# Kernel optimization log

Hardware: AMD Instinct MI355X
Metric: run time of the kernel (lower is better)

The kernel has to match this reference:

```python
import jax, jax.numpy as jnp
import numpy as np
from jax import lax

EPS = 1e-5  # BatchNorm3d default eps


def _dwconv3d(x, w, pad):
    # x: [N,C,D,H,W], w: [C,1,k,k,k] depthwise kernel
    C = w.shape[0]
    return lax.conv_general_dilated(
        x, w,
        window_strides=(1, 1, 1),
        padding=[(pad, pad)] * 3,
        dimension_numbers=('NCDHW', 'OIDHW', 'NCDHW'),
        feature_group_count=C,
    )


def _bn_relu(y, gamma, beta, mean, var):
    # Inference-mode BatchNorm3d folded into a per-channel affine, then ReLU.
    inv = gamma / jnp.sqrt(var + EPS)          # [C]
    scale = inv.reshape(1, -1, 1, 1, 1)
    bias = (beta - mean * inv).reshape(1, -1, 1, 1, 1)
    return jax.nn.relu(y * scale + bias)


def setup_inputs() -> dict:
    key = jax.random.key(0)
    ks = jax.random.split(key, 20)
    C = 32
    x = jax.random.normal(ks[0], (2, C, 64, 128, 128), dtype=jnp.float32)
    w7 = jax.random.normal(ks[1], (C, 1, 7, 7, 7), dtype=jnp.float32) * 0.05
    w3 = jax.random.normal(ks[2], (C, 1, 3, 3, 3), dtype=jnp.float32) * 0.1
    w1 = jax.random.normal(ks[3], (C, 1, 1, 1, 1), dtype=jnp.float32) * 0.3
    def bn_params(i):
        g = jax.random.normal(ks[4 + 4 * i], (C,), dtype=jnp.float32) * 0.1 + 1.0
        b = jax.random.normal(ks[5 + 4 * i], (C,), dtype=jnp.float32) * 0.1
        m = jax.random.normal(ks[6 + 4 * i], (C,), dtype=jnp.float32) * 0.1
        v = jax.random.uniform(ks[7 + 4 * i], (C,), dtype=jnp.float32) + 0.5
        return g, b, m, v
    g7, b7, m7, v7 = bn_params(0)
    g3, b3, m3, v3 = bn_params(1)
    g1, b1, m1, v1 = bn_params(2)
    return dict(x=x, w7=w7, w3=w3, w1=w1,
                g7=g7, b7=b7, m7=m7, v7=v7,
                g3=g3, b3=b3, m3=m3, v3=v3,
                g1=g1, b1=b1, m1=m1, v1=v1)


def reference(x, w7, w3, w1,
              g7, b7, m7, v7,
              g3, b3, m3, v3,
              g1, b1, m1, v1):
    # y = relu(bn7(dw7(x))) + relu(bn3(dw3(x))) + relu(bn1(dw1(x)))
    y = _bn_relu(_dwconv3d(x, w7, 3), g7, b7, m7, v7)
    y = y + _bn_relu(_dwconv3d(x, w3, 1), g3, b3, m3, v3)
    # 1x1x1 depthwise conv == per-channel scalar multiply
    y = y + _bn_relu(x * w1[:, 0, 0, 0, 0].reshape(1, -1, 1, 1, 1), g1, b1, m1, v1)
    return jax.nn.relu(x + y)
```

## Files before the change

kernel.cpp:

```cpp
#include <hip/hip_runtime.h>
#include <hip/hip_bf16.h>

#define Dd 64
#define Hh 128
#define Ww 128
#define Cc 32

#define BD 32
#define BH 16
#define BW 16
#define ZR (BD + 6)
#define HR (BH + 6)
#define NR (ZR * HR)
#define RCOLS 24
#define BLKROW 3
#define NBLK (NR * BLKROW)

#define N7WIN 14
#define N3WIN 10
#define W3BASE (49 * N7WIN)
#define ZENT   (W3BASE + 9 * N3WIN)
#define NENT   (ZENT + 1)

typedef __attribute__((ext_vector_type(8))) short short8;
typedef __attribute__((ext_vector_type(4))) float floatx4;

static __device__ __forceinline__ unsigned short f2bf(float f) {
    unsigned u = __builtin_bit_cast(unsigned, f);
    u += 0x7fffu + ((u >> 16) & 1u);
    return (unsigned short)(u >> 16);
}

static __device__ __forceinline__ unsigned pk2(float a, float b) {
    union { __hip_bfloat162 h; unsigned u; } cv;
    cv.h = __float22bfloat162_rn(make_float2(a, b));
    return cv.u;
}

__global__ __launch_bounds__(256, 3) void replk_mfma(
    const float* __restrict__ x,
    const float* __restrict__ w7, const float* __restrict__ w3, const float* __restrict__ w1,
    const float* __restrict__ g7, const float* __restrict__ b7, const float* __restrict__ m7, const float* __restrict__ v7,
    const float* __restrict__ g3, const float* __restrict__ b3, const float* __restrict__ m3, const float* __restrict__ v3,
    const float* __restrict__ g1, const float* __restrict__ b1, const float* __restrict__ m1, const float* __restrict__ v1,
    float* __restrict__ out)
{
    __shared__ __align__(16) unsigned short tile[NR * RCOLS];
    __shared__ __align__(16) unsigned short wtab[NENT * 8];

    const int tid = threadIdx.x;

    const unsigned lid = blockIdx.x;
    const unsigned nl = (lid & 7u) * 1024u + (lid >> 3);
    const int bx = nl & 127;
    const int slab = nl >> 7;
    const int c = slab & 31;
    const int nb = slab >> 5;
    const int w0 = (bx & 7) * BW;
    const int h0 = ((bx >> 3) & 7) * BH;
    const int d0 = (bx >> 6) * BD;

    const float* xc = x + (size_t)(nb * Cc + c) * (Dd * Hh * Ww);

    for (int e = tid; e < NENT; e += 256) {
        unsigned short h8[8];
#pragma unroll
        for (int j = 0; j < 8; j++) {
            float v = 0.f;
            if (e < W3BASE) {
                int pl = e / N7WIN, a = e - pl * N7WIN;
                int t = a + j - 7;
                if ((unsigned)t < 7u)
                    v = w7[c * 343 + (pl / 7) * 49 + (pl % 7) * 7 + t];
            } else if (e < ZENT) {
                int e2 = e - W3BASE;
                int p3 = e2 / N3WIN, a = e2 - p3 * N3WIN;
                int t = a + j - 7;
                if ((unsigned)t < 3u)
                    v = w3[c * 27 + (p3 / 3) * 9 + (p3 % 3) * 3 + t];
            }
            h8[j] = f2bf(v);
        }
        uint4 pk;
        pk.x = (unsigned)h8[0] | ((unsigned)h8[1] << 16);
        pk.y = (unsigned)h8[2] | ((unsigned)h8[3] << 16);
        pk.z = (unsigned)h8[4] | ((unsigned)h8[5] << 16);
        pk.w = (unsigned)h8[6] | ((unsigned)h8[7] << 16);
        *(uint4*)&wtab[e * 8] = pk;
    }

#pragma unroll
    for (int it = 0; it < 10; it++) {
        int s = tid + it * 256;
        if (s < NBLK) {
            int R = s / BLKROW, bl = s - R * BLKROW;
            int zi = R / HR, hr = R - zi * HR;
            int gz = d0 - 3 + zi, gh = h0 - 3 + hr, gw0 = w0 - 4 + bl * 8;
            float v[8];
#pragma unroll
            for (int j = 0; j < 8; j++) v[j] = 0.f;
            if ((unsigned)gz < (unsigned)Dd && (unsigned)gh < (unsigned)Hh) {
                const float* src = xc + ((size_t)gz * Hh + gh) * Ww + gw0;
                if (gw0 >= 0 && gw0 + 8 <= Ww) {
                    float4 a = *(const float4*)src;
                    float4 b = *(const float4*)(src + 4);
                    v[0] = a.x; v[1] = a.y; v[2] = a.z; v[3] = a.w;
                    v[4] = b.x; v[5] = b.y; v[6] = b.z; v[7] = b.w;
                } else {
#pragma unroll
                    for (int j = 0; j < 8; j++) {
                        int gw = gw0 + j;
                        if ((unsigned)gw < (unsigned)Ww) v[j] = src[j];
                    }
                }
            }
            uint4 pk;
            pk.x = pk2(v[0], v[1]);
            pk.y = pk2(v[2], v[3]);
            pk.z = pk2(v[4], v[5]);
            pk.w = pk2(v[6], v[7]);
            *(uint4*)&tile[R * RCOLS + bl * 8] = pk;
        }
    }

    const float eps = 1e-5f;
    const float iv7 = g7[c] / sqrtf(v7[c] + eps);
    const float bb7 = b7[c] - m7[c] * iv7;
    const float iv3 = g3[c] / sqrtf(v3[c] + eps);
    const float bb3 = b3[c] - m3[c] * iv3;
    const float iv1 = g1[c] / sqrtf(v1[c] + eps);
    const float bb1 = b1[c] - m1[c] * iv1;
    const float s1 = w1[c] * iv1;

    __syncthreads();

    const int lane = tid & 63;
    const int wave = tid >> 6;
    const int q = lane & 15;
    const int p = lane >> 4;
    const int khp = p >> 1;
    const int kb  = p & 1;
    const int ddl = q >> 3;
    const int mwq = q & 7;
    const int zbase = wave * 8;

    const int a7 = 8 * kb - mwq + 6;
    const int a3 = a7 - 2;
    const short8* wf = (const short8*)wtab;

    floatx4 acc7[4][2], acc3[4][2];
#pragma unroll
    for (int i = 0; i < 4; i++)
#pragma unroll
        for (int wh = 0; wh < 2; wh++) { acc7[i][wh] = (floatx4)0.f; acc3[i][wh] = (floatx4)0.f; }

#pragma unroll 1
    for (int khg = 0; khg < 4; khg++) {
        const int kh = 2 * khg + khp;
        const bool ok7 = ((unsigned)a7 < 14u) && (kh <= 6);
        const int cb7 = ok7 ? (kh * 14 + a7 - ddl * 98) : (int)ZENT;
        const int st7 = ok7 ? 98 : 0;
        short8 A7g[8];
#pragma unroll
        for (int rz = 0; rz < 8; rz++) {
            int idx = cb7 + rz * st7;
            if (rz == 0) idx = (ddl == 0 && ok7) ? idx : (int)ZENT;
            if (rz == 7) idx = (ddl == 1 && ok7) ? idx : (int)ZENT;
            A7g[rz] = wf[idx];
        }

        const bool has3 = (khg == 1) || (khg == 2);
        short8 A3g[4] = {};
        if (has3) {
            const int kh3 = 2 * (khg - 1) + khp;
            const bool ok3 = ((unsigned)a3 < 10u) && (kh3 <= 2);
            const int cb3 = ok3 ? (W3BASE + kh3 * 10 + a3 - ddl * 30) : (int)ZENT;
            const int st3 = ok3 ? 30 : 0;
#pragma unroll
            for (int rz = 0; rz < 4; rz++) {
                int idx = cb3 + rz * st3;
                if (rz == 0) idx = (ddl == 0 && ok3) ? idx : (int)ZENT;
                if (rz == 3) idx = (ddl == 1 && ok3) ? idx : (int)ZENT;
                A3g[rz] = wf[idx];
            }
        }

        const int rowadd = (khg == 3) ? 6 : (2 * khg + khp);

#pragma unroll
        for (int zi = 0; zi < 14; zi++) {
            const int R = (zbase + zi) * HR + q + rowadd;
            const unsigned short* bp = &tile[R * RCOLS + 8 * kb];
            short8 B0 = *(const short8*)bp;
            short8 B1 = *(const short8*)(bp + 8);
#pragma unroll
            for (int ddg = 0; ddg < 4; ddg++) {
                const int rz = zi - 2 * ddg;
                if (rz >= 0 && rz < 8) {
                    acc7[ddg][0] = __builtin_amdgcn_mfma_f32_16x16x32_bf16(
                        A7g[rz], B0, acc7[ddg][0], 0, 0, 0);
                    acc7[ddg][1] = __builtin_amdgcn_mfma_f32_16x16x32_bf16(
                        A7g[rz], B1, acc7[ddg][1], 0, 0, 0);
                }
            }
            if (has3) {
#pragma unroll
                for (int ddg = 0; ddg < 4; ddg++) {
                    const int rz3 = zi - 2 - 2 * ddg;
                    if (rz3 >= 0 && rz3 < 4) {
                        acc3[ddg][0] = __builtin_amdgcn_mfma_f32_16x16x32_bf16(
                            A3g[rz3], B0, acc3[ddg][0], 0, 0, 0);
                        acc3[ddg][1] = __builtin_amdgcn_mfma_f32_16x16x32_bf16(
                            A3g[rz3], B1, acc3[ddg][1], 0, 0, 0);
                    }
                }
            }
        }
    }

#pragma unroll
    for (int ddg = 0; ddg < 4; ddg++) {
#pragma unroll
        for (int wh = 0; wh < 2; wh++) {
            const int d = d0 + zbase + 2 * ddg + khp;
            const int Rr = (zbase + 2 * ddg + khp + 3) * HR + (q + 3);
            uint2 u = *(const uint2*)&tile[Rr * RCOLS + 8 * wh + 4 * kb + 4];
            float xr[4];
            xr[0] = __builtin_bit_cast(float, u.x << 16);
            xr[1] = __builtin_bit_cast(float, u.x & 0xffff0000u);
            xr[2] = __builtin_bit_cast(float, u.y << 16);
            xr[3] = __builtin_bit_cast(float, u.y & 0xffff0000u);

            size_t off = ((size_t)(nb * Cc + c) * Dd + d) * (Hh * Ww)
                       + (size_t)(h0 + q) * Ww + w0 + 8 * wh + 4 * kb;
            float o[4];
#pragma unroll
            for (int r = 0; r < 4; r++) {
                float y7 = fmaxf(fmaf(acc7[ddg][wh][r], iv7, bb7), 0.f);
                float y3 = fmaxf(fmaf(acc3[ddg][wh][r], iv3, bb3), 0.f);
                float y1 = fmaxf(fmaf(xr[r], s1, bb1), 0.f);
                o[r] = fmaxf(xr[r] + y7 + y3 + y1, 0.f);
            }
            *(float4*)(out + off) = make_float4(o[0], o[1], o[2], o[3]);
        }
    }
}

extern "C" void kernel_launch(void* const* d_in, const int* in_sizes, int n_in,
                              void* d_out, int out_size, void* d_ws, size_t ws_size,
                              hipStream_t stream) {
    const float* x  = (const float*)d_in[0];
    const float* w7 = (const float*)d_in[1];
    const float* w3 = (const float*)d_in[2];
    const float* w1 = (const float*)d_in[3];
    const float* g7 = (const float*)d_in[4];
    const float* b7 = (const float*)d_in[5];
    const float* m7 = (const float*)d_in[6];
    const float* v7 = (const float*)d_in[7];
    const float* g3 = (const float*)d_in[8];
    const float* b3 = (const float*)d_in[9];
    const float* m3 = (const float*)d_in[10];
    const float* v3 = (const float*)d_in[11];
    const float* g1 = (const float*)d_in[12];
    const float* b1 = (const float*)d_in[13];
    const float* m1 = (const float*)d_in[14];
    const float* v1 = (const float*)d_in[15];
    float* out = (float*)d_out;

    dim3 grid(8192);
    dim3 block(256);
    hipLaunchKernelGGL(replk_mfma, grid, block, 0, stream,
                       x, w7, w3, w1, g7, b7, m7, v7, g3, b3, m3, v3,
                       g1, b1, m1, v1, out);
}
```

Baseline: 260.2 us.

## Split width halves across waves with 512-thread blocks

Doubles the block to 512 threads and splits the two 8-wide column halves of each output tile across separate waves, so each wave keeps half the accumulators and loads one B fragment per row instead of two. The halo tile and weight-table fills use the larger thread count, which shortens the load loops. This cuts register pressure per wave and raises parallelism and occupancy. In exchange, every wave redundantly loads the A weight fragments, and there are more waves per block to schedule around the barrier.

```diff
diff --git a/kernel.cpp b/kernel.cpp
--- a/kernel.cpp
+++ b/kernel.cpp
@@ -37,7 +37,7 @@
     return cv.u;
 }
 
-__global__ __launch_bounds__(256, 3) void replk_mfma(
+__global__ __launch_bounds__(512, 4) void replk_mfma(
     const float* __restrict__ x,
     const float* __restrict__ w7, const float* __restrict__ w3, const float* __restrict__ w1,
     const float* __restrict__ g7, const float* __restrict__ b7, const float* __restrict__ m7, const float* __restrict__ v7,
@@ -62,7 +62,7 @@
 
     const float* xc = x + (size_t)(nb * Cc + c) * (Dd * Hh * Ww);
 
-    for (int e = tid; e < NENT; e += 256) {
+    for (int e = tid; e < NENT; e += 512) {
         unsigned short h8[8];
 #pragma unroll
         for (int j = 0; j < 8; j++) {
@@ -90,8 +90,8 @@
     }
 
 #pragma unroll
-    for (int it = 0; it < 10; it++) {
-        int s = tid + it * 256;
+    for (int it = 0; it < 5; it++) {
+        int s = tid + it * 512;
         if (s < NBLK) {
             int R = s / BLKROW, bl = s - R * BLKROW;
             int zi = R / HR, hr = R - zi * HR;
@@ -136,23 +136,23 @@
 
     const int lane = tid & 63;
     const int wave = tid >> 6;
+    const int whv = wave & 1;
+    const int dgrp = wave >> 1;
     const int q = lane & 15;
     const int p = lane >> 4;
     const int khp = p >> 1;
     const int kb  = p & 1;
     const int ddl = q >> 3;
     const int mwq = q & 7;
-    const int zbase = wave * 8;
+    const int zbase = dgrp * 8;
 
     const int a7 = 8 * kb - mwq + 6;
     const int a3 = a7 - 2;
     const short8* wf = (const short8*)wtab;
 
-    floatx4 acc7[4][2], acc3[4][2];
-#pragma unroll
-    for (int i = 0; i < 4; i++)
-#pragma unroll
-        for (int wh = 0; wh < 2; wh++) { acc7[i][wh] = (floatx4)0.f; acc3[i][wh] = (floatx4)0.f; }
+    floatx4 acc7[4], acc3[4];
+#pragma unroll
+    for (int i = 0; i < 4; i++) { acc7[i] = (floatx4)0.f; acc3[i] = (floatx4)0.f; }
 
 #pragma unroll 1
     for (int khg = 0; khg < 4; khg++) {
@@ -190,29 +190,21 @@
 #pragma unroll
         for (int zi = 0; zi < 14; zi++) {
             const int R = (zbase + zi) * HR + q + rowadd;
-            const unsigned short* bp = &tile[R * RCOLS + 8 * kb];
-            short8 B0 = *(const short8*)bp;
-            short8 B1 = *(const short8*)(bp + 8);
+            short8 B = *(const short8*)&tile[R * RCOLS + 8 * kb + 8 * whv];
 #pragma unroll
             for (int ddg = 0; ddg < 4; ddg++) {
                 const int rz = zi - 2 * ddg;
-                if (rz >= 0 && rz < 8) {
-                    acc7[ddg][0] = __builtin_amdgcn_mfma_f32_16x16x32_bf16(
-                        A7g[rz], B0, acc7[ddg][0], 0, 0, 0);
-                    acc7[ddg][1] = __builtin_amdgcn_mfma_f32_16x16x32_bf16(
-                        A7g[rz], B1, acc7[ddg][1], 0, 0, 0);
-                }
+                if (rz >= 0 && rz < 8)
+                    acc7[ddg] = __builtin_amdgcn_mfma_f32_16x16x32_bf16(
+                        A7g[rz], B, acc7[ddg], 0, 0, 0);
             }
             if (has3) {
 #pragma unroll
                 for (int ddg = 0; ddg < 4; ddg++) {
                     const int rz3 = zi - 2 - 2 * ddg;
-                    if (rz3 >= 0 && rz3 < 4) {
-                        acc3[ddg][0] = __builtin_amdgcn_mfma_f32_16x16x32_bf16(
-                            A3g[rz3], B0, acc3[ddg][0], 0, 0, 0);
-                        acc3[ddg][1] = __builtin_amdgcn_mfma_f32_16x16x32_bf16(
-                            A3g[rz3], B1, acc3[ddg][1], 0, 0, 0);
-                    }
+                    if (rz3 >= 0 && rz3 < 4)
+                        acc3[ddg] = __builtin_amdgcn_mfma_f32_16x16x32_bf16(
+                            A3g[rz3], B, acc3[ddg], 0, 0, 0);
                 }
             }
         }
@@ -220,29 +212,26 @@
 
 #pragma unroll
     for (int ddg = 0; ddg < 4; ddg++) {
-#pragma unroll
-        for (int wh = 0; wh < 2; wh++) {
-            const int d = d0 + zbase + 2 * ddg + khp;
-            const int Rr = (zbase + 2 * ddg + khp + 3) * HR + (q + 3);
-            uint2 u = *(const uint2*)&tile[Rr * RCOLS + 8 * wh + 4 * kb + 4];
-            float xr[4];
-            xr[0] = __builtin_bit_cast(float, u.x << 16);
-            xr[1] = __builtin_bit_cast(float, u.x & 0xffff0000u);
-            xr[2] = __builtin_bit_cast(float, u.y << 16);
-            xr[3] = __builtin_bit_cast(float, u.y & 0xffff0000u);
-
-            size_t off = ((size_t)(nb * Cc + c) * Dd + d) * (Hh * Ww)
-                       + (size_t)(h0 + q) * Ww + w0 + 8 * wh + 4 * kb;
-            float o[4];
-#pragma unroll
-            for (int r = 0; r < 4; r++) {
-                float y7 = fmaxf(fmaf(acc7[ddg][wh][r], iv7, bb7), 0.f);
-                float y3 = fmaxf(fmaf(acc3[ddg][wh][r], iv3, bb3), 0.f);
-                float y1 = fmaxf(fmaf(xr[r], s1, bb1), 0.f);
-                o[r] = fmaxf(xr[r] + y7 + y3 + y1, 0.f);
-            }
-            *(float4*)(out + off) = make_float4(o[0], o[1], o[2], o[3]);
-        }
+        const int d = d0 + zbase + 2 * ddg + khp;
+        const int Rr = (zbase + 2 * ddg + khp + 3) * HR + (q + 3);
+        uint2 u = *(const uint2*)&tile[Rr * RCOLS + 8 * whv + 4 * kb + 4];
+        float xr[4];
+        xr[0] = __builtin_bit_cast(float, u.x << 16);
+        xr[1] = __builtin_bit_cast(float, u.x & 0xffff0000u);
+        xr[2] = __builtin_bit_cast(float, u.y << 16);
+        xr[3] = __builtin_bit_cast(float, u.y & 0xffff0000u);
+
+        size_t off = ((size_t)(nb * Cc + c) * Dd + d) * (Hh * Ww)
+                   + (size_t)(h0 + q) * Ww + w0 + 8 * whv + 4 * kb;
+        float o[4];
+#pragma unroll
+        for (int r = 0; r < 4; r++) {
+            float y7 = fmaxf(fmaf(acc7[ddg][r], iv7, bb7), 0.f);
+            float y3 = fmaxf(fmaf(acc3[ddg][r], iv3, bb3), 0.f);
+            float y1 = fmaxf(fmaf(xr[r], s1, bb1), 0.f);
+            o[r] = fmaxf(xr[r] + y7 + y3 + y1, 0.f);
+        }
+        *(float4*)(out + off) = make_float4(o[0], o[1], o[2], o[3]);
     }
 }
 
@@ -268,7 +257,7 @@
     float* out = (float*)d_out;
 
     dim3 grid(8192);
-    dim3 block(256);
+    dim3 block(512);
     hipLaunchKernelGGL(replk_mfma, grid, block, 0, stream,
                        x, w7, w3, w1, g7, b7, m7, v7, g3, b3, m3, v3,
                        g1, b1, m1, v1, out);
```

New measurement: 252.9 us. 1.03x faster.
